# Kernel optimization log

Hardware: AMD Instinct MI355X
Metric: run time of the kernel (lower is better)

## Reference

```python
import jax, jax.numpy as jnp
import numpy as np

DIVERSITY_WEIGHT = 0.3
UNCERTAINTY_WEIGHT = 0.3
EPS_NORM = 1e-12  # torch F.normalize eps
EPS_LOG = 1e-8


def setup_inputs() -> dict:
    key = jax.random.key(0)
    k1, k2 = jax.random.split(key)
    B, N, D, C = 8, 8192, 512, 2
    x = jax.random.normal(k1, (B, N, D), dtype=jnp.float32)
    c = jax.random.normal(k2, (B, N, C), dtype=jnp.float32)
    return {"x": x, "c": c, "big_lambda": 512}


def reference(x, c, big_lambda):
    B, N, D = x.shape
    C = c.shape[-1]
    big_lambda = min(big_lambda, N)

    # relevance: max class score per instance (C > 1 branch)
    if C == 1:
        relevance = c[..., 0]
    else:
        relevance = jnp.max(c, axis=-1)  # [B, N]

    # diversity: 1 - mean cosine similarity to all other patches.
    # Row-sum of the N x N cosine-sim matrix factorizes:
    #   sum_j xn_i . xn_j = xn_i . (sum_j xn_j)  -> O(N*D) instead of O(N^2*D)
    norms = jnp.linalg.norm(x, axis=-1, keepdims=True)
    x_norm = x / jnp.maximum(norms, EPS_NORM)          # [B, N, D]
    s = jnp.sum(x_norm, axis=1)                        # [B, D]
    row_sums = jnp.einsum('bnd,bd->bn', x_norm, s)     # [B, N]
    avg_sim = (row_sums - 1.0) / (N - 1)
    diversity = 1.0 - avg_sim

    # uncertainty: entropy of class distribution
    if C == 1:
        p = jax.nn.sigmoid(c[..., 0])
        probs = jnp.stack([1.0 - p, p], axis=-1)
    else:
        probs = jax.nn.softmax(c, axis=-1)
    uncertainty = -jnp.sum(probs * jnp.log(probs + EPS_LOG), axis=-1)  # [B, N]

    combined = relevance + DIVERSITY_WEIGHT * diversity + UNCERTAINTY_WEIGHT * uncertainty

    _, selected_indices = jax.lax.top_k(combined, big_lambda)  # [B, big_lambda]
    attention_weights = jax.nn.softmax(combined, axis=1)       # [B, N]
    return selected_indices, attention_weights
```

## Files before the change

kernel.cpp:

```cpp
#include <hip/hip_runtime.h>
#include <stdint.h>

#define B 8
#define N 8192
#define D 512
#define C 2
#define K 512
#define DIV_W 0.3f
#define UNC_W 0.3f

constexpr int ROWS_PER_WAVE  = 16;
constexpr int WAVES_PER_BLK  = 4;
constexpr int ROWS_PER_BLOCK = ROWS_PER_WAVE * WAVES_PER_BLK;
constexpr int BLOCKS_PER_B   = N / ROWS_PER_BLOCK;

__device__ __forceinline__ uint32_t ordmap(float f) {
    uint32_t u = __float_as_uint(f);
    return (u & 0x80000000u) ? ~u : (u | 0x80000000u);
}
__device__ __forceinline__ float ordunmap(uint32_t u) {
    return (u >> 31) ? __uint_as_float(u & 0x7FFFFFFFu) : __uint_as_float(~u);
}

__global__ __launch_bounds__(256) void k_norm_s(const float* __restrict__ x,
                                                float* __restrict__ inv_norm,
                                                float* __restrict__ s) {
    int blk  = blockIdx.x;
    int b    = blk / BLOCKS_PER_B;
    int rb   = (blk % BLOCKS_PER_B) * ROWS_PER_BLOCK;
    int tid  = threadIdx.x;
    int wave = tid >> 6;
    int lane = tid & 63;

    const float4* xb = (const float4*)(x + (size_t)b * N * D);

    float4 accA = {0.f, 0.f, 0.f, 0.f};
    float4 accB = {0.f, 0.f, 0.f, 0.f};

    int row0 = rb + wave * ROWS_PER_WAVE;
    for (int r = 0; r < ROWS_PER_WAVE; ++r) {
        int row = row0 + r;
        const float4* xr = xb + (size_t)row * (D / 4);
        float4 a  = xr[lane];
        float4 bb = xr[64 + lane];

        float ss = a.x*a.x + a.y*a.y + a.z*a.z + a.w*a.w
                 + bb.x*bb.x + bb.y*bb.y + bb.z*bb.z + bb.w*bb.w;
        #pragma unroll
        for (int o = 32; o > 0; o >>= 1) ss += __shfl_xor(ss, o, 64);

        float inv = 1.0f / fmaxf(sqrtf(ss), 1e-12f);
        if (lane == 0) inv_norm[b * N + row] = inv;

        accA.x += a.x * inv;  accA.y += a.y * inv;
        accA.z += a.z * inv;  accA.w += a.w * inv;
        accB.x += bb.x * inv; accB.y += bb.y * inv;
        accB.z += bb.z * inv; accB.w += bb.w * inv;
    }

    __shared__ float sp[WAVES_PER_BLK][D];
    float* dA = &sp[wave][lane * 4];
    dA[0] = accA.x; dA[1] = accA.y; dA[2] = accA.z; dA[3] = accA.w;
    float* dB = &sp[wave][256 + lane * 4];
    dB[0] = accB.x; dB[1] = accB.y; dB[2] = accB.z; dB[3] = accB.w;
    __syncthreads();

    for (int d = tid; d < D; d += 256) {
        float v = sp[0][d] + sp[1][d] + sp[2][d] + sp[3][d];
        atomicAdd(&s[b * D + d], v);
    }
}

__global__ __launch_bounds__(256) void k_combined(const float* __restrict__ x,
                                                  const float* __restrict__ c,
                                                  const float* __restrict__ inv_norm,
                                                  const float* __restrict__ s,
                                                  float* __restrict__ combined) {
    __shared__ float sl[D];
    int blk  = blockIdx.x;
    int b    = blk / BLOCKS_PER_B;
    int rb   = (blk % BLOCKS_PER_B) * ROWS_PER_BLOCK;
    int tid  = threadIdx.x;
    int wave = tid >> 6;
    int lane = tid & 63;

    for (int d = tid; d < D; d += 256) sl[d] = s[b * D + d];
    __syncthreads();

    const float4* sv = (const float4*)sl;
    float4 sA = sv[lane];
    float4 sB = sv[64 + lane];

    const float4* xb = (const float4*)(x + (size_t)b * N * D);
    int row0 = rb + wave * ROWS_PER_WAVE;
    for (int r = 0; r < ROWS_PER_WAVE; ++r) {
        int row = row0 + r;
        const float4* xr = xb + (size_t)row * (D / 4);
        float4 a  = xr[lane];
        float4 bb = xr[64 + lane];

        float dot = a.x*sA.x + a.y*sA.y + a.z*sA.z + a.w*sA.w
                  + bb.x*sB.x + bb.y*sB.y + bb.z*sB.z + bb.w*sB.w;
        #pragma unroll
        for (int o = 32; o > 0; o >>= 1) dot += __shfl_xor(dot, o, 64);

        if (lane == 0) {
            float rs  = dot * inv_norm[b * N + row];
            float div = 1.0f - (rs - 1.0f) / (float)(N - 1);

            const float* cc = c + ((size_t)b * N + row) * C;
            float c0 = cc[0], c1 = cc[1];
            float rel = fmaxf(c0, c1);
            float m  = rel;
            float e0 = expf(c0 - m), e1 = expf(c1 - m);
            float Z  = e0 + e1;
            float p0 = e0 / Z, p1 = e1 / Z;
            float ent = -(p0 * logf(p0 + 1e-8f) + p1 * logf(p1 + 1e-8f));

            combined[b * N + row] = rel + DIV_W * div + UNC_W * ent;
        }
    }
}

__global__ __launch_bounds__(512) void k_topk_sm(const float* __restrict__ combined,
                                                 float* __restrict__ out_idx,
                                                 float* __restrict__ out_w) {
    __shared__ uint32_t vals[N];
    __shared__ float    ex[N];
    __shared__ uint64_t cand[K];
    __shared__ uint32_t hist[256];
    __shared__ uint32_t tiew[256];
    __shared__ uint32_t wred[8];
    __shared__ float    fred[8];
    __shared__ uint32_t sc_prefix, sc_remK, sc_cnt;

    const int b    = blockIdx.x;
    const int tid  = threadIdx.x;
    const int lane = tid & 63;
    const int wave = tid >> 6;
    const float* cb = combined + b * N;

    uint32_t umax = 0;
    const float4* cb4 = (const float4*)cb;
    for (int i4 = tid; i4 < N / 4; i4 += 512) {
        float4 f = cb4[i4];
        uint32_t u0 = ordmap(f.x), u1 = ordmap(f.y);
        uint32_t u2 = ordmap(f.z), u3 = ordmap(f.w);
        uint4 uu; uu.x = u0; uu.y = u1; uu.z = u2; uu.w = u3;
        ((uint4*)vals)[i4] = uu;
        umax = max(umax, max(max(u0, u1), max(u2, u3)));
    }
    #pragma unroll
    for (int o = 32; o > 0; o >>= 1) umax = max(umax, __shfl_xor(umax, o, 64));
    if (lane == 0) wred[wave] = umax;
    if (tid == 0) { sc_remK = K; sc_prefix = 0u; sc_cnt = 0u; }
    __syncthreads();
    uint32_t bmax = wred[0];
    #pragma unroll
    for (int q = 1; q < 8; ++q) bmax = max(bmax, wred[q]);
    const float m = ordunmap(bmax);

    float sum = 0.f;
    for (int i = tid; i < N; i += 512) {
        float e = expf(ordunmap(vals[i]) - m);
        ex[i] = e;
        sum += e;
    }
    #pragma unroll
    for (int o = 32; o > 0; o >>= 1) sum += __shfl_xor(sum, o, 64);
    if (lane == 0) fred[wave] = sum;
    __syncthreads();
    float Z = 0.f;
    #pragma unroll
    for (int q = 0; q < 8; ++q) Z += fred[q];
    const float invZ = 1.0f / Z;
    for (int i = tid; i < N; i += 512)
        out_w[b * N + i] = ex[i] * invZ;

    uint32_t prefix = 0, maskHi = 0;
    for (int p = 3; p >= 0; --p) {
        if (tid < 256) hist[tid] = 0u;
        __syncthreads();
        const int sh = 8 * p;
        for (int i = tid; i < N; i += 512) {
            uint32_t v = vals[i];
            if ((v & maskHi) == prefix)
                atomicAdd(&hist[(v >> sh) & 0xFFu], 1u);
        }
        __syncthreads();
        if (wave == 0) {
            uint32_t c[4], lsum = 0;
            #pragma unroll
            for (int q = 0; q < 4; ++q) { c[q] = hist[lane * 4 + q]; lsum += c[q]; }
            uint32_t ssum = lsum;
            #pragma unroll
            for (int off = 1; off < 64; off <<= 1) {
                uint32_t t2 = __shfl_down(ssum, off, 64);
                if (lane + off < 64) ssum += t2;
            }
            uint32_t cum = ssum - lsum;
            const uint32_t remK = sc_remK;
            #pragma unroll
            for (int q = 3; q >= 0; --q) {
                if (cum < remK && cum + c[q] >= remK) {
                    sc_prefix = prefix | ((uint32_t)(lane * 4 + q) << sh);
                    sc_remK   = remK - cum;
                }
                cum += c[q];
            }
        }
        __syncthreads();
        prefix = sc_prefix;
        maskHi |= (0xFFu << sh);
    }
    const uint32_t T    = prefix;
    const uint32_t remF = sc_remK;

    if (tid < 256) tiew[tid] = 0u;
    __syncthreads();
    for (int i = tid; i < N; i += 512) {
        uint32_t v = vals[i];
        if (v > T) {
            uint32_t slot = atomicAdd(&sc_cnt, 1u);
            cand[slot] = ((uint64_t)v << 13) | (uint32_t)(8191 - i);
        } else if (v == T) {
            atomicOr(&tiew[i >> 5], 1u << (i & 31));
        }
    }
    __syncthreads();
    const uint32_t base = sc_cnt;
    if (wave == 0) {
        const int w0 = lane * 4;
        uint32_t lsum = 0;
        #pragma unroll
        for (int q = 0; q < 4; ++q) lsum += __popc(tiew[w0 + q]);
        uint32_t ssum = lsum;
        #pragma unroll
        for (int off = 1; off < 64; off <<= 1) {
            uint32_t t2 = __shfl_up(ssum, off, 64);
            if (lane >= off) ssum += t2;
        }
        uint32_t rank = ssum - lsum;
        for (int q = 0; q < 4; ++q) {
            uint32_t word = tiew[w0 + q];
            while (word) {
                int bpos = __builtin_ctz(word);
                if (rank < remF) {
                    uint32_t idx = (uint32_t)(w0 + q) * 32u + (uint32_t)bpos;
                    cand[base + rank] = ((uint64_t)T << 13) | (uint32_t)(8191 - idx);
                }
                rank++;
                word &= word - 1;
            }
        }
    }
    __syncthreads();

    uint64_t v = cand[tid];
    __syncthreads();
    for (int k = 2; k <= 512; k <<= 1) {
        for (int j = k >> 1; j > 0; j >>= 1) {
            const bool desc  = ((tid & k) == 0);
            const bool lower = ((tid & j) == 0);
            uint64_t pv;
            if (j >= 64) {
                cand[tid] = v;
                __syncthreads();
                pv = cand[tid ^ j];
                __syncthreads();
            } else {
                pv = __shfl_xor(v, j, 64);
            }
            const bool keepmax = (lower == desc);
            const bool take = keepmax ? (pv > v) : (pv < v);
            if (take) v = pv;
        }
    }
    out_idx[b * K + tid] = (float)(8191u - (uint32_t)(v & 0x1FFFu));
}

extern "C" void kernel_launch(void* const* d_in, const int* in_sizes, int n_in,
                              void* d_out, int out_size, void* d_ws, size_t ws_size,
                              hipStream_t stream) {
    const float* x = (const float*)d_in[0];
    const float* c = (const float*)d_in[1];

    float* ws       = (float*)d_ws;
    float* s        = ws;
    float* inv_norm = s + B * D;
    float* combined = inv_norm + B * N;

    float* out = (float*)d_out;

    hipMemsetAsync(s, 0, B * D * sizeof(float), stream);

    k_norm_s  <<<B * BLOCKS_PER_B, 256, 0, stream>>>(x, inv_norm, s);
    k_combined<<<B * BLOCKS_PER_B, 256, 0, stream>>>(x, c, inv_norm, s, combined);
    k_topk_sm <<<B, 512, 0, stream>>>(combined, out, out + B * K);
}
```

Measured before the change: 81.58 us.

## Replace atomic s accumulation with partials reduce; keep top-k values in registers

The first kernel now writes per-block partial sums of normalized rows, and a new small kernel reduces them into s. This replaces the memset and the global float atomics, and also makes the sum deterministic. The top-k/softmax kernel now runs 1024 threads, each holding 8 values in registers instead of staging all N values and exponentials in shared memory. That cuts LDS traffic and shared-memory footprint, but adds an extra kernel launch and a partials buffer write/read.

```diff
diff --git a/kernel.cpp b/kernel.cpp
--- a/kernel.cpp
+++ b/kernel.cpp
@@ -24,7 +24,7 @@
 
 __global__ __launch_bounds__(256) void k_norm_s(const float* __restrict__ x,
                                                 float* __restrict__ inv_norm,
-                                                float* __restrict__ s) {
+                                                float* __restrict__ partials) {
     int blk  = blockIdx.x;
     int b    = blk / BLOCKS_PER_B;
     int rb   = (blk % BLOCKS_PER_B) * ROWS_PER_BLOCK;
@@ -65,10 +65,20 @@
     dB[0] = accB.x; dB[1] = accB.y; dB[2] = accB.z; dB[3] = accB.w;
     __syncthreads();
 
-    for (int d = tid; d < D; d += 256) {
-        float v = sp[0][d] + sp[1][d] + sp[2][d] + sp[3][d];
-        atomicAdd(&s[b * D + d], v);
-    }
+    float* dst = partials + (size_t)blk * D;
+    for (int d = tid; d < D; d += 256)
+        dst[d] = sp[0][d] + sp[1][d] + sp[2][d] + sp[3][d];
+}
+
+__global__ __launch_bounds__(512) void k_reduce_s(const float* __restrict__ partials,
+                                                  float* __restrict__ s) {
+    int b = blockIdx.x;
+    int d = threadIdx.x;
+    const float* p = partials + (size_t)b * BLOCKS_PER_B * D + d;
+    float acc = 0.f;
+    #pragma unroll 8
+    for (int j = 0; j < BLOCKS_PER_B; ++j) acc += p[(size_t)j * D];
+    s[b * D + d] = acc;
 }
 
 __global__ __launch_bounds__(256) void k_combined(const float* __restrict__ x,
@@ -111,8 +121,7 @@
             const float* cc = c + ((size_t)b * N + row) * C;
             float c0 = cc[0], c1 = cc[1];
             float rel = fmaxf(c0, c1);
-            float m  = rel;
-            float e0 = expf(c0 - m), e1 = expf(c1 - m);
+            float e0 = expf(c0 - rel), e1 = expf(c1 - rel);
             float Z  = e0 + e1;
             float p0 = e0 / Z, p1 = e1 / Z;
             float ent = -(p0 * logf(p0 + 1e-8f) + p1 * logf(p1 + 1e-8f));
@@ -122,34 +131,32 @@
     }
 }
 
-__global__ __launch_bounds__(512) void k_topk_sm(const float* __restrict__ combined,
-                                                 float* __restrict__ out_idx,
-                                                 float* __restrict__ out_w) {
-    __shared__ uint32_t vals[N];
-    __shared__ float    ex[N];
+__global__ __launch_bounds__(1024) void k_topk_sm(const float* __restrict__ combined,
+                                                  float* __restrict__ out_idx,
+                                                  float* __restrict__ out_w) {
     __shared__ uint64_t cand[K];
     __shared__ uint32_t hist[256];
     __shared__ uint32_t tiew[256];
-    __shared__ uint32_t wred[8];
-    __shared__ float    fred[8];
+    __shared__ uint32_t wred[16];
+    __shared__ float    fred[16];
     __shared__ uint32_t sc_prefix, sc_remK, sc_cnt;
 
     const int b    = blockIdx.x;
     const int tid  = threadIdx.x;
     const int lane = tid & 63;
     const int wave = tid >> 6;
-    const float* cb = combined + b * N;
+
+    const float4* cb4 = (const float4*)(combined + b * N);
+    float4 f0 = cb4[tid];
+    float4 f1 = cb4[1024 + tid];
+
+    uint32_t v[8];
+    v[0] = ordmap(f0.x); v[1] = ordmap(f0.y); v[2] = ordmap(f0.z); v[3] = ordmap(f0.w);
+    v[4] = ordmap(f1.x); v[5] = ordmap(f1.y); v[6] = ordmap(f1.z); v[7] = ordmap(f1.w);
 
     uint32_t umax = 0;
-    const float4* cb4 = (const float4*)cb;
-    for (int i4 = tid; i4 < N / 4; i4 += 512) {
-        float4 f = cb4[i4];
-        uint32_t u0 = ordmap(f.x), u1 = ordmap(f.y);
-        uint32_t u2 = ordmap(f.z), u3 = ordmap(f.w);
-        uint4 uu; uu.x = u0; uu.y = u1; uu.z = u2; uu.w = u3;
-        ((uint4*)vals)[i4] = uu;
-        umax = max(umax, max(max(u0, u1), max(u2, u3)));
-    }
+    #pragma unroll
+    for (int q = 0; q < 8; ++q) umax = max(umax, v[q]);
     #pragma unroll
     for (int o = 32; o > 0; o >>= 1) umax = max(umax, __shfl_xor(umax, o, 64));
     if (lane == 0) wred[wave] = umax;
@@ -157,41 +164,42 @@
     __syncthreads();
     uint32_t bmax = wred[0];
     #pragma unroll
-    for (int q = 1; q < 8; ++q) bmax = max(bmax, wred[q]);
+    for (int q = 1; q < 16; ++q) bmax = max(bmax, wred[q]);
     const float m = ordunmap(bmax);
 
+    float e[8];
     float sum = 0.f;
-    for (int i = tid; i < N; i += 512) {
-        float e = expf(ordunmap(vals[i]) - m);
-        ex[i] = e;
-        sum += e;
-    }
+    #pragma unroll
+    for (int q = 0; q < 8; ++q) { e[q] = expf(ordunmap(v[q]) - m); sum += e[q]; }
     #pragma unroll
     for (int o = 32; o > 0; o >>= 1) sum += __shfl_xor(sum, o, 64);
     if (lane == 0) fred[wave] = sum;
     __syncthreads();
     float Z = 0.f;
     #pragma unroll
-    for (int q = 0; q < 8; ++q) Z += fred[q];
+    for (int q = 0; q < 16; ++q) Z += fred[q];
     const float invZ = 1.0f / Z;
-    for (int i = tid; i < N; i += 512)
-        out_w[b * N + i] = ex[i] * invZ;
+    float4* ow = (float4*)(out_w + b * N);
+    float4 w0 = {e[0]*invZ, e[1]*invZ, e[2]*invZ, e[3]*invZ};
+    float4 w1 = {e[4]*invZ, e[5]*invZ, e[6]*invZ, e[7]*invZ};
+    ow[tid]        = w0;
+    ow[1024 + tid] = w1;
 
     uint32_t prefix = 0, maskHi = 0;
     for (int p = 3; p >= 0; --p) {
         if (tid < 256) hist[tid] = 0u;
         __syncthreads();
         const int sh = 8 * p;
-        for (int i = tid; i < N; i += 512) {
-            uint32_t v = vals[i];
-            if ((v & maskHi) == prefix)
-                atomicAdd(&hist[(v >> sh) & 0xFFu], 1u);
+        #pragma unroll
+        for (int q = 0; q < 8; ++q) {
+            if ((v[q] & maskHi) == prefix)
+                atomicAdd(&hist[(v[q] >> sh) & 0xFFu], 1u);
         }
         __syncthreads();
         if (wave == 0) {
-            uint32_t c[4], lsum = 0;
+            uint32_t cc[4], lsum = 0;
             #pragma unroll
-            for (int q = 0; q < 4; ++q) { c[q] = hist[lane * 4 + q]; lsum += c[q]; }
+            for (int q = 0; q < 4; ++q) { cc[q] = hist[lane * 4 + q]; lsum += cc[q]; }
             uint32_t ssum = lsum;
             #pragma unroll
             for (int off = 1; off < 64; off <<= 1) {
@@ -202,11 +210,11 @@
             const uint32_t remK = sc_remK;
             #pragma unroll
             for (int q = 3; q >= 0; --q) {
-                if (cum < remK && cum + c[q] >= remK) {
+                if (cum < remK && cum + cc[q] >= remK) {
                     sc_prefix = prefix | ((uint32_t)(lane * 4 + q) << sh);
                     sc_remK   = remK - cum;
                 }
-                cum += c[q];
+                cum += cc[q];
             }
         }
         __syncthreads();
@@ -218,22 +226,24 @@
 
     if (tid < 256) tiew[tid] = 0u;
     __syncthreads();
-    for (int i = tid; i < N; i += 512) {
-        uint32_t v = vals[i];
-        if (v > T) {
+    #pragma unroll
+    for (int q = 0; q < 8; ++q) {
+        uint32_t idx = (q < 4) ? (uint32_t)(4 * tid + q)
+                               : (uint32_t)(4096 + 4 * tid + (q - 4));
+        if (v[q] > T) {
             uint32_t slot = atomicAdd(&sc_cnt, 1u);
-            cand[slot] = ((uint64_t)v << 13) | (uint32_t)(8191 - i);
-        } else if (v == T) {
-            atomicOr(&tiew[i >> 5], 1u << (i & 31));
+            cand[slot] = ((uint64_t)v[q] << 13) | (uint32_t)(8191 - idx);
+        } else if (v[q] == T) {
+            atomicOr(&tiew[idx >> 5], 1u << (idx & 31));
         }
     }
     __syncthreads();
     const uint32_t base = sc_cnt;
     if (wave == 0) {
-        const int w0 = lane * 4;
+        const int w0i = lane * 4;
         uint32_t lsum = 0;
         #pragma unroll
-        for (int q = 0; q < 4; ++q) lsum += __popc(tiew[w0 + q]);
+        for (int q = 0; q < 4; ++q) lsum += __popc(tiew[w0i + q]);
         uint32_t ssum = lsum;
         #pragma unroll
         for (int off = 1; off < 64; off <<= 1) {
@@ -242,11 +252,11 @@
         }
         uint32_t rank = ssum - lsum;
         for (int q = 0; q < 4; ++q) {
-            uint32_t word = tiew[w0 + q];
+            uint32_t word = tiew[w0i + q];
             while (word) {
                 int bpos = __builtin_ctz(word);
                 if (rank < remF) {
-                    uint32_t idx = (uint32_t)(w0 + q) * 32u + (uint32_t)bpos;
+                    uint32_t idx = (uint32_t)(w0i + q) * 32u + (uint32_t)bpos;
                     cand[base + rank] = ((uint64_t)T << 13) | (uint32_t)(8191 - idx);
                 }
                 rank++;
@@ -256,27 +266,27 @@
     }
     __syncthreads();
 
-    uint64_t v = cand[tid];
-    __syncthreads();
-    for (int k = 2; k <= 512; k <<= 1) {
+    uint64_t sv = (tid < K) ? cand[tid] : 0ULL;
+    __syncthreads();
+    for (int k = 2; k <= K; k <<= 1) {
         for (int j = k >> 1; j > 0; j >>= 1) {
             const bool desc  = ((tid & k) == 0);
             const bool lower = ((tid & j) == 0);
             uint64_t pv;
             if (j >= 64) {
-                cand[tid] = v;
+                if (tid < K) cand[tid] = sv;
                 __syncthreads();
-                pv = cand[tid ^ j];
+                pv = (tid < K) ? cand[tid ^ j] : 0ULL;
                 __syncthreads();
             } else {
-                pv = __shfl_xor(v, j, 64);
+                pv = __shfl_xor(sv, j, 64);
             }
             const bool keepmax = (lower == desc);
-            const bool take = keepmax ? (pv > v) : (pv < v);
-            if (take) v = pv;
-        }
-    }
-    out_idx[b * K + tid] = (float)(8191u - (uint32_t)(v & 0x1FFFu));
+            if (tid < K && (keepmax ? (pv > sv) : (pv < sv))) sv = pv;
+        }
+    }
+    if (tid < K)
+        out_idx[b * K + tid] = (float)(8191u - (uint32_t)(sv & 0x1FFFu));
 }
 
 extern "C" void kernel_launch(void* const* d_in, const int* in_sizes, int n_in,
@@ -286,15 +296,15 @@
     const float* c = (const float*)d_in[1];
 
     float* ws       = (float*)d_ws;
-    float* s        = ws;
+    float* partials = ws;
+    float* s        = partials + B * BLOCKS_PER_B * D;
     float* inv_norm = s + B * D;
     float* combined = inv_norm + B * N;
 
     float* out = (float*)d_out;
 
-    hipMemsetAsync(s, 0, B * D * sizeof(float), stream);
-
-    k_norm_s  <<<B * BLOCKS_PER_B, 256, 0, stream>>>(x, inv_norm, s);
+    k_norm_s  <<<B * BLOCKS_PER_B, 256, 0, stream>>>(x, inv_norm, partials);
+    k_reduce_s<<<B, 512, 0, stream>>>(partials, s);
     k_combined<<<B * BLOCKS_PER_B, 256, 0, stream>>>(x, c, inv_norm, s, combined);
-    k_topk_sm <<<B, 512, 0, stream>>>(combined, out, out + B * K);
-}
+    k_topk_sm <<<B, 1024, 0, stream>>>(combined, out, out + B * K);
+}
```

Measured after the change: 78.43 us. 3.9% less time.
